# Kernel tuning notes

Hardware: AMD Instinct MI355X
Metric: run time of the kernel (lower is better)

## Reference

```python
import jax, jax.numpy as jnp
import numpy as np

N = 100000   # nodes
E = 3200000  # edges (avg degree 32)
G = 512      # graphs in batch
F_IN = 10
H = 30


def setup_inputs() -> dict:
    key = jax.random.key(0)
    ks = jax.random.split(key, 14)
    x = jax.random.normal(ks[0], (N, F_IN), dtype=jnp.float32)
    edge_index = jax.random.randint(ks[1], (2, E), 0, N, dtype=jnp.int64)
    batch = jnp.sort(jax.random.randint(ks[2], (N,), 0, G, dtype=jnp.int64))
    edge_weights = jnp.ones((E,), dtype=jnp.float32)
    s = 0.1
    W1 = jax.random.normal(ks[3], (F_IN, H), jnp.float32) * s
    b1 = jnp.zeros((H,), jnp.float32)
    W2 = jax.random.normal(ks[4], (H, H), jnp.float32) * s
    b2 = jnp.zeros((H,), jnp.float32)
    W3 = jax.random.normal(ks[5], (H, H), jnp.float32) * s
    b3 = jnp.zeros((H,), jnp.float32)
    LW1 = jax.random.normal(ks[6], (H, 10), jnp.float32) * s
    Lb1 = jnp.zeros((10,), jnp.float32)
    LW2 = jax.random.normal(ks[7], (10, 2), jnp.float32) * s
    Lb2 = jnp.zeros((2,), jnp.float32)
    return dict(x=x, edge_index=edge_index, batch=batch, edge_weights=edge_weights,
                W1=W1, b1=b1, W2=W2, b2=b2, W3=W3, b3=b3,
                LW1=LW1, Lb1=Lb1, LW2=LW2, Lb2=Lb2)


def reference(x, edge_index, batch, edge_weights, W1, b1, W2, b2, W3, b3, LW1, Lb1, LW2, Lb2):
    n = x.shape[0]
    row, col = edge_index[0], edge_index[1]
    # PyG gcn_norm: add self-loops with weight 1, symmetric normalization
    loop = jnp.arange(n)
    row_f = jnp.concatenate([row, loop])
    col_f = jnp.concatenate([col, loop])
    w_f = jnp.concatenate([edge_weights, jnp.ones((n,), edge_weights.dtype)])
    deg = jax.ops.segment_sum(w_f, col_f, num_segments=n)
    dis = jnp.where(deg > 0, jax.lax.rsqrt(jnp.where(deg > 0, deg, 1.0)), 0.0)
    norm = dis[row_f] * w_f * dis[col_f]  # [E+N]

    def gcn(h, W, b):
        h = h @ W  # [N, out]
        agg = jax.ops.segment_sum(norm[:, None] * h[row_f], col_f, num_segments=n)
        return agg + b

    h = jax.nn.relu(gcn(x, W1, b1))
    h = jax.nn.relu(gcn(h, W2, b2))
    h = jax.nn.relu(gcn(h, W3, b3))  # embedding [N, 30]
    pooled = jax.ops.segment_max(h, batch, num_segments=G)  # [G, 30]
    out = jax.nn.relu(pooled @ LW1 + Lb1) @ LW2 + Lb2  # [G, 2]
    return out
```

## Files before the change

kernel.cpp:

```cpp
#include <hip/hip_runtime.h>
#include <hip/hip_bf16.h>


#define WG 256
#define CAP 9216
#define T_EDGES 16384

__global__ void k_init(int* bcur, float* pooled, int nb16, int pooledN) {
    int i = blockIdx.x * blockDim.x + threadIdx.x;
    if (i < nb16) bcur[i] = 0;
    if (i < pooledN) pooled[i] = 0.0f;
}

__global__ __launch_bounds__(1024)
void k_bucket(const int* __restrict__ row, const int* __restrict__ col,
              const float* __restrict__ w,
              int* bcur, int2* __restrict__ buck, int E, int NB) {
    __shared__ int hist[512];
    __shared__ int base[512];
    int tid = threadIdx.x;
    for (int i = tid; i < NB; i += 1024) hist[i] = 0;
    __syncthreads();
    int start = blockIdx.x * T_EDGES;
    int end = min(start + T_EDGES, E);
    for (int i = start + tid; i < end; i += 1024)
        atomicAdd(&hist[col[i] >> 8], 1);
    __syncthreads();
    for (int i = tid; i < NB; i += 1024) {
        int h = hist[i];
        base[i] = (h > 0) ? atomicAdd(&bcur[i * 16], h) : 0;
        hist[i] = 0;
    }
    __syncthreads();
    for (int i = start + tid; i < end; i += 1024) {
        int c = col[i];
        int b = c >> 8;
        int off = atomicAdd(&hist[b], 1);
        int pos = base[b] + off;
        if (pos < CAP) {
            int2 pk;
            pk.x = (c & 255) | (row[i] << 8);
            pk.y = __float_as_int(w[i]);
            buck[(size_t)b * CAP + pos] = pk;
        }
    }
}

__global__ __launch_bounds__(512)
void k_scanb(const int* __restrict__ bcur, int* __restrict__ bbase,
             int* __restrict__ ptr, int NB, int N) {
    __shared__ int sh[512];
    int t = threadIdx.x;
    int v = (t < NB) ? min(bcur[t * 16], CAP) : 0;
    sh[t] = v;
    __syncthreads();
    for (int off = 1; off < 512; off <<= 1) {
        int tt = (t >= off) ? sh[t - off] : 0;
        __syncthreads();
        sh[t] += tt;
        __syncthreads();
    }
    if (t < NB) bbase[t] = sh[t] - v;
    if (t == 511) ptr[N] = sh[511];
}

__global__ __launch_bounds__(1024)
void k_fuse(const int* __restrict__ bcur, const int2* __restrict__ buck,
            const int* __restrict__ bbase,
            float* __restrict__ dis, int* __restrict__ ptr,
            int2* __restrict__ csr, int N) {
    __shared__ int lc[256];
    __shared__ float lw[256];
    __shared__ int sh[256];
    __shared__ int cur[256];
    int b = blockIdx.x;
    int tid = threadIdx.x;
    if (tid < 256) { lc[tid] = 0; lw[tid] = 0.0f; }
    __syncthreads();
    int m = min(bcur[b * 16], CAP);
    const int2* bp = buck + (size_t)b * CAP;
    for (int i = tid; i < m; i += 1024) {
        int2 pk = bp[i];
        int lcol = pk.x & 255;
        atomicAdd(&lc[lcol], 1);
        atomicAdd(&lw[lcol], __int_as_float(pk.y));
    }
    __syncthreads();
    int lcnt = 0;
    if (tid < 256) { lcnt = lc[tid]; sh[tid] = lcnt; }
    __syncthreads();
    for (int off = 1; off < 256; off <<= 1) {
        int t = (tid >= off && tid < 256) ? sh[tid - off] : 0;
        __syncthreads();
        if (tid < 256) sh[tid] += t;
        __syncthreads();
    }
    int node = (b << 8) + tid;
    if (tid < 256) {
        int base = bbase[b] + sh[tid] - lcnt;
        cur[tid] = base;
        if (node < N) {
            ptr[node] = base;
            float d = 1.0f + lw[tid];
            dis[node] = (d > 0.0f) ? (1.0f / sqrtf(d)) : 0.0f;
        }
    }
    __syncthreads();
    for (int i = tid; i < m; i += 1024) {
        int2 pk = bp[i];
        int lcol = pk.x & 255;
        int pos = atomicAdd(&cur[lcol], 1);
        int2 rec;
        rec.x = (int)(((unsigned)pk.x) >> 8);
        rec.y = pk.y;
        csr[pos] = rec;
    }
}

template <int K>
__global__ void k_matmul(const float* __restrict__ in, int in_stride,
                         const float* __restrict__ W, const float* __restrict__ dis,
                         float* __restrict__ out, int n) {
    __shared__ float Ws[K * 30];
    for (int idx = threadIdx.x; idx < K * 30; idx += blockDim.x) Ws[idx] = W[idx];
    __syncthreads();
    int gid = blockIdx.x * blockDim.x + threadIdx.x;
    int node = gid >> 5;
    int f = gid & 31;
    if (node < n) {
        float acc = 0.0f;
        if (f < 30) {
            const float* ip = in + (size_t)node * in_stride;
#pragma unroll
            for (int k = 0; k < K; k++) acc += ip[k] * Ws[k * 30 + f];
            acc *= dis[node];
        }
        out[(size_t)node * 32 + f] = acc;
    }
}

__global__ void k_agg(const float* __restrict__ hw, const float* __restrict__ dis,
                      const int* __restrict__ ptr, const int2* __restrict__ csr,
                      const float* __restrict__ bias,
                      float* __restrict__ out, int n) {
    int wid = (blockIdx.x * blockDim.x + threadIdx.x) >> 6;
    int lane = threadIdx.x & 63;
    if (wid >= n) return;
    int f = lane & 31;
    int half = lane >> 5;
    int s = ptr[wid];
    int e = ptr[wid + 1];
    float acc = 0.0f;
    for (int base = s; base < e; base += 32) {
        int idxv = 0; float nrmv = 0.0f;
        int src = base + lane;
        if (lane < 32 && src < e) {
            int2 v = csr[src];
            idxv = v.x;
            nrmv = __int_as_float(v.y);
        }
#pragma unroll
        for (int j = 0; j < 16; j++) {
            int sl = 2 * j + half;
            int r = __shfl(idxv, sl, 64);
            float w = __shfl(nrmv, sl, 64);
            acc += w * hw[(size_t)r * 32 + f];
        }
    }
    acc += __shfl_xor(acc, 32, 64);
    float dc = dis[wid];
    float r = dc * (acc + hw[(size_t)wid * 32 + f]);
    if (half == 0 && f < 30) {
        r += bias[f];
        out[(size_t)wid * 32 + f] = fmaxf(r, 0.0f);
    }
}

__global__ void k_pool(const float* __restrict__ h, const int* __restrict__ batch,
                       float* pooled, int n) {
    int gid = blockIdx.x * blockDim.x + threadIdx.x;
    int chunk = gid >> 5;
    int f = gid & 31;
    int n0 = chunk * 64;
    if (n0 >= n || f >= 30) return;
    int end = min(n0 + 64, n);
    int curg = batch[n0];
    float m = 0.0f;
    for (int i = n0; i < end; i++) {
        int g = batch[i];
        if (g != curg) {
            atomicMax((int*)&pooled[curg * 32 + f], __float_as_int(m));
            m = 0.0f;
            curg = g;
        }
        m = fmaxf(m, h[(size_t)i * 32 + f]);
    }
    atomicMax((int*)&pooled[curg * 32 + f], __float_as_int(m));
}

__global__ void k_mlp(const float* __restrict__ pooled,
                      const float* __restrict__ LW1, const float* __restrict__ Lb1,
                      const float* __restrict__ LW2, const float* __restrict__ Lb2,
                      float* __restrict__ out, int G) {
    int g = blockIdx.x * blockDim.x + threadIdx.x;
    if (g >= G) return;
    float p[30];
#pragma unroll
    for (int k = 0; k < 30; k++) p[k] = pooled[g * 32 + k];
    float o0 = Lb2[0], o1 = Lb2[1];
#pragma unroll
    for (int j = 0; j < 10; j++) {
        float hj = Lb1[j];
#pragma unroll
        for (int k = 0; k < 30; k++) hj += p[k] * LW1[k * 10 + j];
        hj = fmaxf(hj, 0.0f);
        o0 += hj * LW2[j * 2 + 0];
        o1 += hj * LW2[j * 2 + 1];
    }
    out[g * 2 + 0] = o0;
    out[g * 2 + 1] = o1;
}

extern "C" void kernel_launch(void* const* d_in, const int* in_sizes, int n_in,
                              void* d_out, int out_size, void* d_ws, size_t ws_size,
                              hipStream_t stream) {
    const float* x     = (const float*)d_in[0];
    const int*   ei    = (const int*)d_in[1];
    const int*   batch = (const int*)d_in[2];
    const float* ew    = (const float*)d_in[3];
    const float* W1 = (const float*)d_in[4];  const float* b1  = (const float*)d_in[5];
    const float* W2 = (const float*)d_in[6];  const float* b2  = (const float*)d_in[7];
    const float* W3 = (const float*)d_in[8];  const float* b3  = (const float*)d_in[9];
    const float* LW1 = (const float*)d_in[10]; const float* Lb1 = (const float*)d_in[11];
    const float* LW2 = (const float*)d_in[12]; const float* Lb2 = (const float*)d_in[13];
    float* out = (float*)d_out;

    const int N = in_sizes[2];
    const int E = in_sizes[3];
    const int G = out_size / 2;
    const int* row = ei;
    const int* col = ei + E;

    const int NB = (N + 255) >> 8;

    char* p = (char*)d_ws;
    auto carve = [&](size_t bytes) -> void* {
        void* r = (void*)p;
        p += (bytes + 255) & ~(size_t)255;
        return r;
    };
    int*   ptr       = (int*)carve((size_t)(N + 1) * 4);
    float* dis       = (float*)carve((size_t)N * 4);
    int*   bcur      = (int*)carve((size_t)NB * 16 * 4);
    int*   bbase     = (int*)carve((size_t)NB * 4);
    int2*  csr       = (int2*)carve((size_t)E * 8);
    size_t buckBytes = (size_t)NB * CAP * 8;
    size_t featBytes = (size_t)N * 32 * 4 * 2;
    char*  regionA   = (char*)carve(buckBytes > featBytes ? buckBytes : featBytes);
    int2*  buck      = (int2*)regionA;
    float* bufW      = (float*)regionA;
    float* bufH      = (float*)(regionA + (size_t)N * 32 * 4);
    float* pooled    = (float*)carve((size_t)G * 32 * 4);

    int initN = (NB * 16 > G * 32) ? NB * 16 : G * 32;

    k_init<<<(initN + WG - 1) / WG, WG, 0, stream>>>(bcur, pooled, NB * 16, G * 32);
    k_bucket<<<(E + T_EDGES - 1) / T_EDGES, 1024, 0, stream>>>(row, col, ew, bcur, buck, E, NB);
    k_scanb<<<1, 512, 0, stream>>>(bcur, bbase, ptr, NB, N);
    k_fuse<<<NB, 1024, 0, stream>>>(bcur, buck, bbase, dis, ptr, csr, N);

    int mm_grid  = (int)(((size_t)N * 32 + WG - 1) / WG);
    int agg_grid = (int)(((size_t)N * 64 + WG - 1) / WG);

    k_matmul<10><<<mm_grid, WG, 0, stream>>>(x, 10, W1, dis, bufW, N);
    k_agg<<<agg_grid, WG, 0, stream>>>(bufW, dis, ptr, csr, b1, bufH, N);
    k_matmul<30><<<mm_grid, WG, 0, stream>>>(bufH, 32, W2, dis, bufW, N);
    k_agg<<<agg_grid, WG, 0, stream>>>(bufW, dis, ptr, csr, b2, bufH, N);
    k_matmul<30><<<mm_grid, WG, 0, stream>>>(bufH, 32, W3, dis, bufW, N);
    k_agg<<<agg_grid, WG, 0, stream>>>(bufW, dis, ptr, csr, b3, bufH, N);

    int pool_grid = (int)((((size_t)(N + 63) / 64) * 32 + WG - 1) / WG);
    k_pool<<<pool_grid, WG, 0, stream>>>(bufH, batch, pooled, N);
    k_mlp<<<(G + WG - 1) / WG, WG, 0, stream>>>(pooled, LW1, Lb1, LW2, Lb2, out, G);
}
```

Measured before the change: 445.3 us.

## Fuse next-layer matmul into aggregation and fold bucket scan into CSR build

Each of the first two GCN aggregations now applies bias and ReLU, then multiplies by the next layer's weight matrix inside the same wavefront using shuffles. This removes two separate matmul launches and the write and re-read of the intermediate features. The separate single-block scan kernel is also removed: every k_fuse block recomputes the 512-entry bucket prefix sum in shared memory. That saves a launch and a global round trip at the cost of redundant scans and extra syncs in every block.

```diff
diff --git a/kernel.cpp b/kernel.cpp
--- a/kernel.cpp
+++ b/kernel.cpp
@@ -46,38 +46,29 @@
     }
 }
 
-__global__ __launch_bounds__(512)
-void k_scanb(const int* __restrict__ bcur, int* __restrict__ bbase,
-             int* __restrict__ ptr, int NB, int N) {
-    __shared__ int sh[512];
-    int t = threadIdx.x;
-    int v = (t < NB) ? min(bcur[t * 16], CAP) : 0;
-    sh[t] = v;
-    __syncthreads();
-    for (int off = 1; off < 512; off <<= 1) {
-        int tt = (t >= off) ? sh[t - off] : 0;
-        __syncthreads();
-        sh[t] += tt;
-        __syncthreads();
-    }
-    if (t < NB) bbase[t] = sh[t] - v;
-    if (t == 511) ptr[N] = sh[511];
-}
-
 __global__ __launch_bounds__(1024)
 void k_fuse(const int* __restrict__ bcur, const int2* __restrict__ buck,
-            const int* __restrict__ bbase,
             float* __restrict__ dis, int* __restrict__ ptr,
-            int2* __restrict__ csr, int N) {
+            int2* __restrict__ csr, int N, int NB) {
     __shared__ int lc[256];
     __shared__ float lw[256];
     __shared__ int sh[256];
     __shared__ int cur[256];
+    __shared__ int sb[512];
     int b = blockIdx.x;
     int tid = threadIdx.x;
+    if (tid < 512) sb[tid] = (tid < NB) ? min(bcur[tid * 16], CAP) : 0;
     if (tid < 256) { lc[tid] = 0; lw[tid] = 0.0f; }
     __syncthreads();
+    for (int off = 1; off < 512; off <<= 1) {
+        int v = (tid < 512 && tid >= off) ? sb[tid - off] : 0;
+        __syncthreads();
+        if (tid < 512) sb[tid] += v;
+        __syncthreads();
+    }
     int m = min(bcur[b * 16], CAP);
+    int bbase = sb[b] - m;
+    if (b == 0 && tid == 0) ptr[N] = sb[511];
     const int2* bp = buck + (size_t)b * CAP;
     for (int i = tid; i < m; i += 1024) {
         int2 pk = bp[i];
@@ -97,7 +88,7 @@
     }
     int node = (b << 8) + tid;
     if (tid < 256) {
-        int base = bbase[b] + sh[tid] - lcnt;
+        int base = bbase + sh[tid] - lcnt;
         cur[tid] = base;
         if (node < N) {
             ptr[node] = base;
@@ -137,6 +128,58 @@
         }
         out[(size_t)node * 32 + f] = acc;
     }
+}
+
+__global__ void k_agg_fused(const float* __restrict__ hw, const float* __restrict__ dis,
+                            const int* __restrict__ ptr, const int2* __restrict__ csr,
+                            const float* __restrict__ bias, const float* __restrict__ Wn,
+                            float* __restrict__ outw, int n) {
+    __shared__ float Ws[30 * 32];
+    for (int idx = threadIdx.x; idx < 30 * 32; idx += blockDim.x) {
+        int rr = idx >> 5, cc = idx & 31;
+        Ws[idx] = (cc < 30) ? Wn[rr * 30 + cc] : 0.0f;
+    }
+    __syncthreads();
+    int wid = (blockIdx.x * blockDim.x + threadIdx.x) >> 6;
+    int lane = threadIdx.x & 63;
+    if (wid >= n) return;
+    int f = lane & 31;
+    int half = lane >> 5;
+    int s = ptr[wid];
+    int e = ptr[wid + 1];
+    float acc = 0.0f;
+    for (int base = s; base < e; base += 32) {
+        int idxv = 0; float nrmv = 0.0f;
+        int src = base + lane;
+        if (lane < 32 && src < e) {
+            int2 v = csr[src];
+            idxv = v.x;
+            nrmv = __int_as_float(v.y);
+        }
+#pragma unroll
+        for (int j = 0; j < 16; j++) {
+            int sl = 2 * j + half;
+            int r = __shfl(idxv, sl, 64);
+            float w = __shfl(nrmv, sl, 64);
+            acc += w * hw[(size_t)r * 32 + f];
+        }
+    }
+    acc += __shfl_xor(acc, 32, 64);
+    float dc = dis[wid];
+    float r = dc * (acc + hw[(size_t)wid * 32 + f]);
+    float bf = (f < 30) ? bias[f] : 0.0f;
+    float h = fmaxf(r + bf, 0.0f);
+    if (f >= 30) h = 0.0f;
+    float o = 0.0f;
+#pragma unroll
+    for (int k = 0; k < 15; k++) {
+        int kk = half * 15 + k;
+        float rk = __shfl(h, kk, 64);
+        o += rk * Ws[kk * 32 + f];
+    }
+    o += __shfl_xor(o, 32, 64);
+    o *= dc;
+    if (half == 0) outw[(size_t)wid * 32 + f] = o;
 }
 
 __global__ void k_agg(const float* __restrict__ hw, const float* __restrict__ dis,
@@ -252,7 +295,6 @@
     int*   ptr       = (int*)carve((size_t)(N + 1) * 4);
     float* dis       = (float*)carve((size_t)N * 4);
     int*   bcur      = (int*)carve((size_t)NB * 16 * 4);
-    int*   bbase     = (int*)carve((size_t)NB * 4);
     int2*  csr       = (int2*)carve((size_t)E * 8);
     size_t buckBytes = (size_t)NB * CAP * 8;
     size_t featBytes = (size_t)N * 32 * 4 * 2;
@@ -266,17 +308,14 @@
 
     k_init<<<(initN + WG - 1) / WG, WG, 0, stream>>>(bcur, pooled, NB * 16, G * 32);
     k_bucket<<<(E + T_EDGES - 1) / T_EDGES, 1024, 0, stream>>>(row, col, ew, bcur, buck, E, NB);
-    k_scanb<<<1, 512, 0, stream>>>(bcur, bbase, ptr, NB, N);
-    k_fuse<<<NB, 1024, 0, stream>>>(bcur, buck, bbase, dis, ptr, csr, N);
+    k_fuse<<<NB, 1024, 0, stream>>>(bcur, buck, dis, ptr, csr, N, NB);
 
     int mm_grid  = (int)(((size_t)N * 32 + WG - 1) / WG);
     int agg_grid = (int)(((size_t)N * 64 + WG - 1) / WG);
 
     k_matmul<10><<<mm_grid, WG, 0, stream>>>(x, 10, W1, dis, bufW, N);
-    k_agg<<<agg_grid, WG, 0, stream>>>(bufW, dis, ptr, csr, b1, bufH, N);
-    k_matmul<30><<<mm_grid, WG, 0, stream>>>(bufH, 32, W2, dis, bufW, N);
-    k_agg<<<agg_grid, WG, 0, stream>>>(bufW, dis, ptr, csr, b2, bufH, N);
-    k_matmul<30><<<mm_grid, WG, 0, stream>>>(bufH, 32, W3, dis, bufW, N);
+    k_agg_fused<<<agg_grid, WG, 0, stream>>>(bufW, dis, ptr, csr, b1, W2, bufH, N);
+    k_agg_fused<<<agg_grid, WG, 0, stream>>>(bufH, dis, ptr, csr, b2, W3, bufW, N);
     k_agg<<<agg_grid, WG, 0, stream>>>(bufW, dis, ptr, csr, b3, bufH, N);
 
     int pool_grid = (int)((((size_t)(N + 63) / 64) * 32 + WG - 1) / WG);
```

New measurement: 440.8 us. Within noise of the previous version (-1.0%).
